# Performance work log

Measured on AMD Instinct MI355X. Metric: run time of the kernel, lower is better.

Reference implementation:

```python
import jax, jax.numpy as jnp
import numpy as np

ENT_SIZE = 250000
REL_SIZE = 64
EMBED = 128
B = 32768
K = 8


def setup_inputs() -> dict:
    key = jax.random.key(0)
    ks = jax.random.split(key, 9)
    initrange = 0.5 / EMBED
    u = lambda k, n: jax.random.uniform(k, (n, EMBED), jnp.float32, -initrange, initrange)
    V = ENT_SIZE + REL_SIZE  # unified vocab: entities first, then relations
    return {
        "in_ent_w": u(ks[0], ENT_SIZE),
        "out_ent_w": u(ks[1], ENT_SIZE),
        "in_rel_w": u(ks[2], REL_SIZE),
        "out_rel_w": u(ks[3], REL_SIZE),
        "in_map_w": u(ks[4], REL_SIZE),
        "out_map_w": u(ks[5], REL_SIZE),
        "input_labels": jax.random.randint(ks[6], (B,), 0, V, jnp.int32),
        "pos_labels": jax.random.randint(ks[7], (B,), 0, V, jnp.int32),
        "neg_labels": jax.random.randint(ks[8], (B, K), 0, V, jnp.int32),
    }


def _map(ent, mapping):
    # project ent onto the hyperplane normal to normalize(mapping)  (TransH-style)
    n = mapping / jnp.maximum(jnp.linalg.norm(mapping, axis=-1, keepdims=True), 1e-12)
    return ent - jnp.sum(ent * n, axis=-1, keepdims=True) * n


def _pair_embs(iid, pid, is_ent_i, is_ent_p, in_ent_w, out_ent_w, in_rel_w, out_rel_w, in_map_w, out_map_w):
    """Per-row (input_emb, output_emb) per the 4 mask branches, plus the stable
    permutation that reproduces torch's boolean-mask + concat row ordering."""
    rel_size = in_rel_w.shape[0]
    iid_r = jnp.minimum(iid, rel_size - 1)  # clip: only used where label is a relation
    pid_r = jnp.minimum(pid, rel_size - 1)
    e_in = in_ent_w[iid]        # [N, D]
    r_in = in_rel_w[iid_r]
    e_out = out_ent_w[pid]
    r_out = out_rel_w[pid_r]
    mp_in = in_map_w[pid_r]
    mp_out = out_map_w[iid_r]
    mi = is_ent_i[:, None]
    mp = is_ent_p[:, None]
    inp = jnp.where(mi, jnp.where(mp, e_in, _map(e_in, mp_in)), r_in)
    out = jnp.where(mp, jnp.where(mi, e_out, _map(e_out, mp_out)), r_out)
    # branch key: 0=(ent,ent) 1=(ent,rel) 2=(rel,ent) 3=(rel,rel) -> concat order
    branch = (~is_ent_i).astype(jnp.int32) * 2 + (~is_ent_p).astype(jnp.int32)
    perm = jnp.argsort(branch, stable=True)
    return inp[perm], out[perm]


def reference(in_ent_w, out_ent_w, in_rel_w, out_rel_w, in_map_w, out_map_w,
              input_labels, pos_labels, neg_labels):
    ent_size = in_ent_w.shape[0]
    b, k = neg_labels.shape
    neg_flat = neg_labels.reshape(-1)

    # reverse_id_map: entity labels keep id, relation labels offset by ent_size
    to_id = lambda lab: jnp.where(lab < ent_size, lab, lab - ent_size)
    is_ent = lambda lab: lab < ent_size

    iid, pid, nid = to_id(input_labels), to_id(pos_labels), to_id(neg_flat)
    ii, ip, inn = is_ent(input_labels), is_ent(pos_labels), is_ent(neg_flat)

    Ws = (in_ent_w, out_ent_w, in_rel_w, out_rel_w, in_map_w, out_map_w)

    inp_pos, out_pos = _pair_embs(iid, pid, ii, ip, *Ws)
    iid_rep = jnp.repeat(iid, k)
    ii_rep = jnp.repeat(ii, k)
    inp_neg, out_neg = _pair_embs(iid_rep, nid, ii_rep, inn, *Ws)

    log_pos = jax.nn.log_sigmoid(jnp.sum(out_pos * inp_pos, axis=-1))          # [B]
    log_neg = jax.nn.log_sigmoid(jnp.sum(out_neg * (-inp_neg), axis=-1))       # [B*K]
    log_neg = log_neg.reshape(b, k).sum(axis=1)                                # [B]
    return -(log_pos + log_neg)
```

## Files before the change

### kernel.cpp

```cpp
#include <hip/hip_runtime.h>
#include <hip/hip_bf16.h>
#include <stdint.h>

#define ENT 250000
#define RELSZ 64
#define D 128
#define BATCH 32768
#define KNEG 8


__device__ __forceinline__ float logsig(float x) {
  return fminf(x, 0.f) - log1pf(expf(-fabsf(x)));
}

__global__ void k_prep(const float* __restrict__ in_rel, const float* __restrict__ out_rel,
                       const float* __restrict__ in_map, const float* __restrict__ out_map,
                       const int* __restrict__ in_lab, const int* __restrict__ pos_lab,
                       const int* __restrict__ neg_lab,
                       float* __restrict__ t1, float* __restrict__ t2, float* __restrict__ RR,
                       int* __restrict__ C, uint16_t* __restrict__ rank_pos,
                       uint16_t* __restrict__ rank_neg, float* __restrict__ out) {
  __shared__ float ls[4];
  __shared__ float sri[2][128];
  __shared__ int wc[4][4];
  int blk = blockIdx.x, t = threadIdx.x;

  if (blk >= 1152) {
    int sub = t >> 7, tt = t & 127;
    int p = (blk - 1152) * 2 + sub;
    float im = in_map[p * D + tt], om = out_map[p * D + tt];
    float ro = out_rel[p * D + tt], ri = in_rel[p * D + tt];
    float v, r;
    float n_im, n_om;
    v = im * im;
#pragma unroll
    for (int off = 32; off > 0; off >>= 1) v += __shfl_xor(v, off, 64);
    if ((t & 63) == 0) ls[t >> 6] = v;
    __syncthreads();
    r = ls[sub * 2] + ls[sub * 2 + 1];
    n_im = im / fmaxf(sqrtf(r), 1e-12f);
    __syncthreads();
    v = om * om;
#pragma unroll
    for (int off = 32; off > 0; off >>= 1) v += __shfl_xor(v, off, 64);
    if ((t & 63) == 0) ls[t >> 6] = v;
    __syncthreads();
    r = ls[sub * 2] + ls[sub * 2 + 1];
    n_om = om / fmaxf(sqrtf(r), 1e-12f);
    __syncthreads();
    v = n_im * ro;
#pragma unroll
    for (int off = 32; off > 0; off >>= 1) v += __shfl_xor(v, off, 64);
    if ((t & 63) == 0) ls[t >> 6] = v;
    __syncthreads();
    float d1 = ls[sub * 2] + ls[sub * 2 + 1];
    __syncthreads();
    v = n_om * ri;
#pragma unroll
    for (int off = 32; off > 0; off >>= 1) v += __shfl_xor(v, off, 64);
    if ((t & 63) == 0) ls[t >> 6] = v;
    __syncthreads();
    float d2 = ls[sub * 2] + ls[sub * 2 + 1];
    t1[p * D + tt] = ro - d1 * n_im;
    t2[p * D + tt] = ri - d2 * n_om;
    sri[sub][tt] = ri;
    __syncthreads();
    int half = t >> 7, lq = t & 127;
    if (lq < RELSZ) {
      int pr = (blk - 1152) * 2 + half;
      const float* rq = out_rel + lq * D;
      const float* s = sri[half];
      float acc = 0.f;
#pragma unroll 8
      for (int d = 0; d < D; d += 4) {
        float4 r4 = *(const float4*)(rq + d);
        acc += s[d] * r4.x + s[d + 1] * r4.y + s[d + 2] * r4.z + s[d + 3] * r4.w;
      }
      RR[pr * RELSZ + lq] = acc;
    }
    return;
  }

  int wave = t >> 6, lane = t & 63;
  int key, i;
  bool is_pos = blk < 128;
  if (is_pos) {
    i = blk * 256 + t;
    int il = in_lab[i], pl = pos_lab[i];
    key = ((il >= ENT) ? 2 : 0) | ((pl >= ENT) ? 1 : 0);
  } else {
    i = (blk - 128) * 256 + t;
    int il = in_lab[i >> 3], nl = neg_lab[i];
    key = ((il >= ENT) ? 2 : 0) | ((nl >= ENT) ? 1 : 0);
  }
  unsigned long long m[4];
#pragma unroll
  for (int v = 0; v < 4; v++) m[v] = __ballot(key == v);
  if (lane < 4) wc[wave][lane] = __popcll(m[lane]);
  int wrank = __popcll(m[key] & ((1ull << lane) - 1ull));
  __syncthreads();
  if (t < 4) {
    int s = wc[0][t] + wc[1][t] + wc[2][t] + wc[3][t];
    int idx = is_pos ? (t * 128 + blk) : (512 + t * 1024 + (blk - 128));
    C[idx] = s;
  }
  int wpre = 0;
  for (int w = 0; w < wave; w++) wpre += wc[w][key];
  uint16_t rk = (uint16_t)(wpre + wrank);
  if (is_pos) { rank_pos[i] = rk; out[i] = 0.f; }
  else        { rank_neg[i] = rk; }
}

__global__ void k_scan(int* __restrict__ C) {
  int t = threadIdx.x, lane = t & 63, w = t >> 6;
  int base = t * 18;
  int v[18];
  int s = 0;
#pragma unroll
  for (int j = 0; j < 18; j++) { v[j] = C[base + j]; s += v[j]; }
  int inc = s;
#pragma unroll
  for (int off = 1; off < 64; off <<= 1) {
    int x = __shfl_up(inc, off, 64);
    if (lane >= off) inc += x;
  }
  __shared__ int wsum[4];
  if (lane == 63) wsum[w] = inc;
  __syncthreads();
  int wpre = 0;
  for (int i = 0; i < w; i++) wpre += wsum[i];
  int run = wpre + inc - s;
#pragma unroll
  for (int j = 0; j < 18; j++) { C[base + j] = run; run += v[j]; }
}

__global__ void k_main(const float* __restrict__ in_ent, const float* __restrict__ out_ent,
                       const float* __restrict__ t1, const float* __restrict__ t2,
                       const float* __restrict__ RR,
                       const int* __restrict__ in_lab, const int* __restrict__ pos_lab,
                       const int* __restrict__ neg_lab,
                       const int* __restrict__ C, const uint16_t* __restrict__ rank_pos,
                       const uint16_t* __restrict__ rank_neg, float* __restrict__ out) {
  int b = __builtin_amdgcn_readfirstlane((int)((blockIdx.x * blockDim.x + threadIdx.x) >> 6));
  int lane = threadIdx.x & 63;
  int q = lane & 7, g = lane >> 3;

  int il = in_lab[b];
  bool ei = il < ENT;
  int iid = ei ? il : il - ENT;
  const float* Lp = (ei ? in_ent + (size_t)iid * D : t2 + (size_t)iid * D) + q * 4;
  float4 L0 = *(const float4*)(Lp);
  float4 L1 = *(const float4*)(Lp + 32);
  float4 L2 = *(const float4*)(Lp + 64);
  float4 L3 = *(const float4*)(Lp + 96);

  int oA = (g == 0) ? pos_lab[b] : neg_lab[b * 8 + g - 1];
  int oB = neg_lab[b * 8 + 7];
  int keyA = (ei ? 0 : 2) | ((oA < ENT) ? 0 : 1);
  int keyB = (ei ? 0 : 2) | ((oB < ENT) ? 0 : 1);

  int dA = 0, dB = 0;
  if (q == 0) {
    if (g == 0) {
      dA = C[keyA * 128 + (b >> 8)] + (int)rank_pos[b];
    } else {
      int i = b * 8 + g - 1;
      dA = (C[512 + keyA * 1024 + (i >> 8)] + (int)rank_neg[i] - BATCH) >> 3;
    }
    if (g == 7) {
      int i = b * 8 + 7;
      dB = (C[512 + keyB * 1024 + (i >> 8)] + (int)rank_neg[i] - BATCH) >> 3;
    }
  }

  bool eA = oA < ENT; int oidA = eA ? oA : oA - ENT;
  const float* RpA = (eA ? out_ent + (size_t)oidA * D : t1 + (size_t)oidA * D) + q * 4;
  float4 A0 = *(const float4*)(RpA);
  float4 A1 = *(const float4*)(RpA + 32);
  float4 A2 = *(const float4*)(RpA + 64);
  float4 A3 = *(const float4*)(RpA + 96);

  bool eB = oB < ENT; int oidB = eB ? oB : oB - ENT;
  const float* RpB = (eB ? out_ent + (size_t)oidB * D : t1 + (size_t)oidB * D) + q * 4;
  float4 B0 = *(const float4*)(RpB);
  float4 B1 = *(const float4*)(RpB + 32);
  float4 B2 = *(const float4*)(RpB + 64);
  float4 B3 = *(const float4*)(RpB + 96);

  float pA = L0.x * A0.x + L0.y * A0.y + L0.z * A0.z + L0.w * A0.w +
             L1.x * A1.x + L1.y * A1.y + L1.z * A1.z + L1.w * A1.w +
             L2.x * A2.x + L2.y * A2.y + L2.z * A2.z + L2.w * A2.w +
             L3.x * A3.x + L3.y * A3.y + L3.z * A3.z + L3.w * A3.w;
  float pB = L0.x * B0.x + L0.y * B0.y + L0.z * B0.z + L0.w * B0.w +
             L1.x * B1.x + L1.y * B1.y + L1.z * B1.z + L1.w * B1.w +
             L2.x * B2.x + L2.y * B2.y + L2.z * B2.z + L2.w * B2.w +
             L3.x * B3.x + L3.y * B3.y + L3.z * B3.z + L3.w * B3.w;
#pragma unroll
  for (int off = 4; off > 0; off >>= 1) {
    pA += __shfl_xor(pA, off, 64);
    pB += __shfl_xor(pB, off, 64);
  }

  if (q == 0) {
    float dotA = pA;
    if (!ei && oA >= ENT) dotA = RR[iid * RELSZ + (oA - ENT)];
    float vA = (g == 0) ? logsig(dotA) : logsig(-dotA);
    atomicAdd(out + dA, -vA);
    if (g == 7) {
      float dotB = pB;
      if (!ei && oB >= ENT) dotB = RR[iid * RELSZ + (oB - ENT)];
      atomicAdd(out + dB, -logsig(-dotB));
    }
  }
}

extern "C" void kernel_launch(void* const* d_in, const int* in_sizes, int n_in,
                              void* d_out, int out_size, void* d_ws, size_t ws_size,
                              hipStream_t stream) {
  const float* in_ent  = (const float*)d_in[0];
  const float* out_ent = (const float*)d_in[1];
  const float* in_rel  = (const float*)d_in[2];
  const float* out_rel = (const float*)d_in[3];
  const float* in_map  = (const float*)d_in[4];
  const float* out_map = (const float*)d_in[5];
  const int* in_lab  = (const int*)d_in[6];
  const int* pos_lab = (const int*)d_in[7];
  const int* neg_lab = (const int*)d_in[8];

  char* ws = (char*)d_ws;
  float*    t1       = (float*)(ws + 0);
  float*    t2       = (float*)(ws + 32768);
  float*    RR       = (float*)(ws + 65536);
  int*      C        = (int*)(ws + 81920);
  uint16_t* rank_pos = (uint16_t*)(ws + 100352);
  uint16_t* rank_neg = (uint16_t*)(ws + 165888);
  float*    out      = (float*)d_out;

  k_prep<<<1184, 256, 0, stream>>>(in_rel, out_rel, in_map, out_map,
                                   in_lab, pos_lab, neg_lab,
                                   t1, t2, RR, C, rank_pos, rank_neg, out);
  k_scan<<<1, 256, 0, stream>>>(C);
  k_main<<<8192, 256, 0, stream>>>(in_ent, out_ent, t1, t2, RR,
                                   in_lab, pos_lab, neg_lab,
                                   C, rank_pos, rank_neg, out);
}
```

Measured before the change: 46.74 us.

## Fold scan into prep via last-block counter and split main into per-pair waves

```diff
diff --git a/kernel.cpp b/kernel.cpp
--- a/kernel.cpp
+++ b/kernel.cpp
@@ -19,10 +19,13 @@
                        const int* __restrict__ neg_lab,
                        float* __restrict__ t1, float* __restrict__ t2, float* __restrict__ RR,
                        int* __restrict__ C, uint16_t* __restrict__ rank_pos,
-                       uint16_t* __restrict__ rank_neg, float* __restrict__ out) {
+                       uint16_t* __restrict__ rank_neg, float* __restrict__ out,
+                       int* __restrict__ counter) {
   __shared__ float ls[4];
   __shared__ float sri[2][128];
   __shared__ int wc[4][4];
+  __shared__ int wsum[4];
+  __shared__ int amLast;
   int blk = blockIdx.x, t = threadIdx.x;
 
   if (blk >= 1152) {
@@ -30,8 +33,7 @@
     int p = (blk - 1152) * 2 + sub;
     float im = in_map[p * D + tt], om = out_map[p * D + tt];
     float ro = out_rel[p * D + tt], ri = in_rel[p * D + tt];
-    float v, r;
-    float n_im, n_om;
+    float v, r, n_im, n_om;
     v = im * im;
 #pragma unroll
     for (int off = 32; off > 0; off >>= 1) v += __shfl_xor(v, off, 64);
@@ -78,60 +80,64 @@
       }
       RR[pr * RELSZ + lq] = acc;
     }
-    return;
+  } else {
+    int wave = t >> 6, lane = t & 63;
+    int key, i;
+    bool is_pos = blk < 128;
+    if (is_pos) {
+      i = blk * 256 + t;
+      int il = in_lab[i], pl = pos_lab[i];
+      key = ((il >= ENT) ? 2 : 0) | ((pl >= ENT) ? 1 : 0);
+    } else {
+      i = (blk - 128) * 256 + t;
+      int il = in_lab[i >> 3], nl = neg_lab[i];
+      key = ((il >= ENT) ? 2 : 0) | ((nl >= ENT) ? 1 : 0);
+    }
+    unsigned long long m[4];
+#pragma unroll
+    for (int v = 0; v < 4; v++) m[v] = __ballot(key == v);
+    if (lane < 4) wc[wave][lane] = __popcll(m[lane]);
+    int wrank = __popcll(m[key] & ((1ull << lane) - 1ull));
+    __syncthreads();
+    if (t < 4) {
+      int s = wc[0][t] + wc[1][t] + wc[2][t] + wc[3][t];
+      int idx = is_pos ? (t * 128 + blk) : (512 + t * 1024 + (blk - 128));
+      C[idx] = s;
+    }
+    int wpre = 0;
+    for (int w = 0; w < wave; w++) wpre += wc[w][key];
+    uint16_t rk = (uint16_t)(wpre + wrank);
+    if (is_pos) { rank_pos[i] = rk; out[i] = 0.f; }
+    else        { rank_neg[i] = rk; }
   }
 
-  int wave = t >> 6, lane = t & 63;
-  int key, i;
-  bool is_pos = blk < 128;
-  if (is_pos) {
-    i = blk * 256 + t;
-    int il = in_lab[i], pl = pos_lab[i];
-    key = ((il >= ENT) ? 2 : 0) | ((pl >= ENT) ? 1 : 0);
-  } else {
-    i = (blk - 128) * 256 + t;
-    int il = in_lab[i >> 3], nl = neg_lab[i];
-    key = ((il >= ENT) ? 2 : 0) | ((nl >= ENT) ? 1 : 0);
+  __syncthreads();
+  __threadfence();
+  if (t == 0) amLast = (atomicAdd(counter, 1) == 1184 - 1) ? 1 : 0;
+  __syncthreads();
+  if (!amLast) return;
+  __threadfence();
+  {
+    int lane = t & 63, w = t >> 6;
+    int base = t * 18;
+    int v[18];
+    int s = 0;
+#pragma unroll
+    for (int j = 0; j < 18; j++) { v[j] = C[base + j]; s += v[j]; }
+    int inc = s;
+#pragma unroll
+    for (int off = 1; off < 64; off <<= 1) {
+      int x = __shfl_up(inc, off, 64);
+      if (lane >= off) inc += x;
+    }
+    if (lane == 63) wsum[w] = inc;
+    __syncthreads();
+    int wpre = 0;
+    for (int i2 = 0; i2 < w; i2++) wpre += wsum[i2];
+    int run = wpre + inc - s;
+#pragma unroll
+    for (int j = 0; j < 18; j++) { C[base + j] = run; run += v[j]; }
   }
-  unsigned long long m[4];
-#pragma unroll
-  for (int v = 0; v < 4; v++) m[v] = __ballot(key == v);
-  if (lane < 4) wc[wave][lane] = __popcll(m[lane]);
-  int wrank = __popcll(m[key] & ((1ull << lane) - 1ull));
-  __syncthreads();
-  if (t < 4) {
-    int s = wc[0][t] + wc[1][t] + wc[2][t] + wc[3][t];
-    int idx = is_pos ? (t * 128 + blk) : (512 + t * 1024 + (blk - 128));
-    C[idx] = s;
-  }
-  int wpre = 0;
-  for (int w = 0; w < wave; w++) wpre += wc[w][key];
-  uint16_t rk = (uint16_t)(wpre + wrank);
-  if (is_pos) { rank_pos[i] = rk; out[i] = 0.f; }
-  else        { rank_neg[i] = rk; }
-}
-
-__global__ void k_scan(int* __restrict__ C) {
-  int t = threadIdx.x, lane = t & 63, w = t >> 6;
-  int base = t * 18;
-  int v[18];
-  int s = 0;
-#pragma unroll
-  for (int j = 0; j < 18; j++) { v[j] = C[base + j]; s += v[j]; }
-  int inc = s;
-#pragma unroll
-  for (int off = 1; off < 64; off <<= 1) {
-    int x = __shfl_up(inc, off, 64);
-    if (lane >= off) inc += x;
-  }
-  __shared__ int wsum[4];
-  if (lane == 63) wsum[w] = inc;
-  __syncthreads();
-  int wpre = 0;
-  for (int i = 0; i < w; i++) wpre += wsum[i];
-  int run = wpre + inc - s;
-#pragma unroll
-  for (int j = 0; j < 18; j++) { C[base + j] = run; run += v[j]; }
 }
 
 __global__ void k_main(const float* __restrict__ in_ent, const float* __restrict__ out_ent,
@@ -141,76 +147,53 @@
                        const int* __restrict__ neg_lab,
                        const int* __restrict__ C, const uint16_t* __restrict__ rank_pos,
                        const uint16_t* __restrict__ rank_neg, float* __restrict__ out) {
-  int b = __builtin_amdgcn_readfirstlane((int)((blockIdx.x * blockDim.x + threadIdx.x) >> 6));
-  int lane = threadIdx.x & 63;
+  int blk = blockIdx.x, t = threadIdx.x;
+  int wave = t >> 6, lane = t & 63;
   int q = lane & 7, g = lane >> 3;
 
-  int il = in_lab[b];
+  bool is_pos = blk < 1024;
+  int w = is_pos ? (blk * 4 + wave) : ((blk - 1024) * 4 + wave);
+  int i = w * 8 + g;
+
+  int il, o;
+  if (is_pos) { il = in_lab[i]; o = pos_lab[i]; }
+  else        { il = in_lab[w]; o = neg_lab[i]; }
   bool ei = il < ENT;
   int iid = ei ? il : il - ENT;
+  bool eo = o < ENT;
+  int oid = eo ? o : o - ENT;
+  int key = (ei ? 0 : 2) | (eo ? 0 : 1);
+
+  int rk = is_pos ? (int)rank_pos[i] : (int)rank_neg[i];
+  int cidx = is_pos ? (key * 128 + (i >> 8)) : (512 + key * 1024 + (i >> 8));
+  int cbase = C[cidx];
+
   const float* Lp = (ei ? in_ent + (size_t)iid * D : t2 + (size_t)iid * D) + q * 4;
+  const float* Rp = (eo ? out_ent + (size_t)oid * D : t1 + (size_t)oid * D) + q * 4;
   float4 L0 = *(const float4*)(Lp);
   float4 L1 = *(const float4*)(Lp + 32);
   float4 L2 = *(const float4*)(Lp + 64);
   float4 L3 = *(const float4*)(Lp + 96);
-
-  int oA = (g == 0) ? pos_lab[b] : neg_lab[b * 8 + g - 1];
-  int oB = neg_lab[b * 8 + 7];
-  int keyA = (ei ? 0 : 2) | ((oA < ENT) ? 0 : 1);
-  int keyB = (ei ? 0 : 2) | ((oB < ENT) ? 0 : 1);
-
-  int dA = 0, dB = 0;
+  float4 R0 = *(const float4*)(Rp);
+  float4 R1 = *(const float4*)(Rp + 32);
+  float4 R2 = *(const float4*)(Rp + 64);
+  float4 R3 = *(const float4*)(Rp + 96);
+
+  float p = L0.x * R0.x + L0.y * R0.y + L0.z * R0.z + L0.w * R0.w +
+            L1.x * R1.x + L1.y * R1.y + L1.z * R1.z + L1.w * R1.w +
+            L2.x * R2.x + L2.y * R2.y + L2.z * R2.z + L2.w * R2.w +
+            L3.x * R3.x + L3.y * R3.y + L3.z * R3.z + L3.w * R3.w;
+#pragma unroll
+  for (int off = 4; off > 0; off >>= 1) p += __shfl_xor(p, off, 64);
+
   if (q == 0) {
-    if (g == 0) {
-      dA = C[keyA * 128 + (b >> 8)] + (int)rank_pos[b];
-    } else {
-      int i = b * 8 + g - 1;
-      dA = (C[512 + keyA * 1024 + (i >> 8)] + (int)rank_neg[i] - BATCH) >> 3;
-    }
-    if (g == 7) {
-      int i = b * 8 + 7;
-      dB = (C[512 + keyB * 1024 + (i >> 8)] + (int)rank_neg[i] - BATCH) >> 3;
-    }
-  }
-
-  bool eA = oA < ENT; int oidA = eA ? oA : oA - ENT;
-  const float* RpA = (eA ? out_ent + (size_t)oidA * D : t1 + (size_t)oidA * D) + q * 4;
-  float4 A0 = *(const float4*)(RpA);
-  float4 A1 = *(const float4*)(RpA + 32);
-  float4 A2 = *(const float4*)(RpA + 64);
-  float4 A3 = *(const float4*)(RpA + 96);
-
-  bool eB = oB < ENT; int oidB = eB ? oB : oB - ENT;
-  const float* RpB = (eB ? out_ent + (size_t)oidB * D : t1 + (size_t)oidB * D) + q * 4;
-  float4 B0 = *(const float4*)(RpB);
-  float4 B1 = *(const float4*)(RpB + 32);
-  float4 B2 = *(const float4*)(RpB + 64);
-  float4 B3 = *(const float4*)(RpB + 96);
-
-  float pA = L0.x * A0.x + L0.y * A0.y + L0.z * A0.z + L0.w * A0.w +
-             L1.x * A1.x + L1.y * A1.y + L1.z * A1.z + L1.w * A1.w +
-             L2.x * A2.x + L2.y * A2.y + L2.z * A2.z + L2.w * A2.w +
-             L3.x * A3.x + L3.y * A3.y + L3.z * A3.z + L3.w * A3.w;
-  float pB = L0.x * B0.x + L0.y * B0.y + L0.z * B0.z + L0.w * B0.w +
-             L1.x * B1.x + L1.y * B1.y + L1.z * B1.z + L1.w * B1.w +
-             L2.x * B2.x + L2.y * B2.y + L2.z * B2.z + L2.w * B2.w +
-             L3.x * B3.x + L3.y * B3.y + L3.z * B3.z + L3.w * B3.w;
-#pragma unroll
-  for (int off = 4; off > 0; off >>= 1) {
-    pA += __shfl_xor(pA, off, 64);
-    pB += __shfl_xor(pB, off, 64);
-  }
-
-  if (q == 0) {
-    float dotA = pA;
-    if (!ei && oA >= ENT) dotA = RR[iid * RELSZ + (oA - ENT)];
-    float vA = (g == 0) ? logsig(dotA) : logsig(-dotA);
-    atomicAdd(out + dA, -vA);
-    if (g == 7) {
-      float dotB = pB;
-      if (!ei && oB >= ENT) dotB = RR[iid * RELSZ + (oB - ENT)];
-      atomicAdd(out + dB, -logsig(-dotB));
-    }
+    float dot = p;
+    if (!ei && !eo) dot = RR[iid * RELSZ + oid];
+    int dest;
+    float val;
+    if (is_pos) { dest = cbase + rk;                 val = logsig(dot); }
+    else        { dest = (cbase + rk - BATCH) >> 3;  val = logsig(-dot); }
+    atomicAdd(out + dest, -val);
   }
 }
 
@@ -234,13 +217,14 @@
   int*      C        = (int*)(ws + 81920);
   uint16_t* rank_pos = (uint16_t*)(ws + 100352);
   uint16_t* rank_neg = (uint16_t*)(ws + 165888);
+  int*      counter  = (int*)(ws + 690176);
   float*    out      = (float*)d_out;
 
+  hipMemsetAsync(counter, 0, 4, stream);
   k_prep<<<1184, 256, 0, stream>>>(in_rel, out_rel, in_map, out_map,
                                    in_lab, pos_lab, neg_lab,
-                                   t1, t2, RR, C, rank_pos, rank_neg, out);
-  k_scan<<<1, 256, 0, stream>>>(C);
-  k_main<<<8192, 256, 0, stream>>>(in_ent, out_ent, t1, t2, RR,
+                                   t1, t2, RR, C, rank_pos, rank_neg, out, counter);
+  k_main<<<9216, 256, 0, stream>>>(in_ent, out_ent, t1, t2, RR,
                                    in_lab, pos_lab, neg_lab,
                                    C, rank_pos, rank_neg, out);
 }
```

After: 121.9 us. 2.61x slower.
